# Optimization experiments

Hardware: AMD Instinct MI355X
Metric: run time of the kernel (lower is better)

The kernel has to match this reference:

```python
import jax, jax.numpy as jnp
import numpy as np

G = 32        # grid points per axis (in_p is a regular [0,1]^3 grid)
M = 8         # half n_modes (n_modes=16 -> keep 8 low + 8 high per dim, 8 in rfft dim)
NL = 4        # fno_n_layers
HID = 64      # fno_hidden_channels
LIFT = 256    # fno_lifting_channels
NOUT = 16384  # number of output query points
RADIUS = 0.033


def setup_inputs() -> dict:
    key = jax.random.key(0)
    ks = jax.random.split(key, 16)
    g = jnp.linspace(0.0, 1.0, G)
    X, Y, Z = jnp.meshgrid(g, g, g, indexing='ij')
    in_p = jnp.stack([X, Y, Z], -1).astype(jnp.float32)            # [G,G,G,3]
    f = jax.random.normal(ks[0], (G, G, G, 3), jnp.float32)        # [G,G,G,3]
    out_p = jax.random.uniform(ks[1], (NOUT, 3), dtype=jnp.float32)

    def lin(k, i, o):
        return jax.random.normal(k, (i, o), jnp.float32) * (float(i) ** -0.5)

    inp = {
        'in_p': in_p, 'out_p': out_p, 'f': f,
        # Lifting MLP: (in_channels+3)=6 -> 256 -> 64
        'lift_w1': lin(ks[2], 6, LIFT), 'lift_b1': jnp.zeros((LIFT,), jnp.float32),
        'lift_w2': lin(ks[3], LIFT, HID), 'lift_b2': jnp.zeros((HID,), jnp.float32),
        # Spectral weights: [layer, corner(4), in, out, M, M, M, (re,im)]
        'spec_w': jax.random.normal(ks[4], (NL, 4, HID, HID, M, M, M, 2), jnp.float32) * 0.02,
        # Linear (soft) skip per layer
        'skip_w': jax.random.normal(ks[5], (NL, HID, HID), jnp.float32) * (float(HID) ** -0.5),
        'skip_b': jnp.zeros((NL, HID), jnp.float32),
        # GNO kernel MLP: 6 -> 512 -> 256 -> 64
        'gno_w1': lin(ks[6], 6, 512), 'gno_b1': jnp.zeros((512,), jnp.float32),
        'gno_w2': lin(ks[7], 512, 256), 'gno_b2': jnp.zeros((256,), jnp.float32),
        'gno_w3': lin(ks[8], 256, HID), 'gno_b3': jnp.zeros((HID,), jnp.float32),
        # Projection: 64 -> 256 -> 1
        'proj_w1': lin(ks[9], HID, 256), 'proj_b1': jnp.zeros((256,), jnp.float32),
        'proj_w2': lin(ks[10], 256, 1), 'proj_b2': jnp.zeros((1,), jnp.float32),
    }
    return inp


def reference(in_p, out_p, f, lift_w1, lift_b1, lift_w2, lift_b2, spec_w,
              skip_w, skip_b, gno_w1, gno_b1, gno_w2, gno_b2, gno_w3, gno_b3,
              proj_w1, proj_b1, proj_w2, proj_b2):
    gelu = lambda x: jax.nn.gelu(x, approximate=False)

    # ---- FNO latent embedding (channels-last) ----
    h = jnp.concatenate([f, in_p], -1)                               # [G,G,G,6]
    h = gelu(h @ lift_w1 + lift_b1) @ lift_w2 + lift_b2              # [G,G,G,HID]

    w = spec_w[..., 0] + 1j * spec_w[..., 1]                         # [NL,4,i,o,M,M,M]
    lo, hi = slice(0, M), slice(-M, None)
    corners = [(lo, lo), (lo, hi), (hi, lo), (hi, hi)]
    sz = slice(0, M)
    for l in range(NL):
        ft = jnp.fft.rfftn(h, axes=(0, 1, 2), norm='forward')        # [G,G,G//2+1,HID]
        out_ft = jnp.zeros_like(ft)
        for c, (sx, sy) in enumerate(corners):
            blk = jnp.einsum('xyzi,ioxyz->xyzo', ft[sx, sy, sz], w[l, c])
            out_ft = out_ft.at[sx, sy, sz].set(blk)
        hs = jnp.fft.irfftn(out_ft, s=(G, G, G), axes=(0, 1, 2), norm='forward')
        h = hs + h @ skip_w[l] + skip_b[l]
        if l < NL - 1:
            h = gelu(h)
    latent = h.reshape(-1, HID)                                      # [G^3, HID]

    # ---- GNO: radius neighbor search on regular grid + gather-MLP-mean ----
    hgrid = 1.0 / (G - 1)
    i0 = jnp.round(out_p * (G - 1)).astype(jnp.int32)                # nearest cell [N,3]
    off = jnp.stack(jnp.meshgrid(*([jnp.arange(-1, 2)] * 3), indexing='ij'), -1).reshape(-1, 3)
    cand = i0[:, None, :] + off[None]                                # [N,27,3]
    inb = jnp.all((cand >= 0) & (cand < G), -1)
    cc = jnp.clip(cand, 0, G - 1)
    flat = (cc[..., 0] * G + cc[..., 1]) * G + cc[..., 2]            # [N,27]
    ycoord = cc.astype(jnp.float32) * hgrid                          # neighbor coords
    d2 = jnp.sum((out_p[:, None, :] - ycoord) ** 2, -1)
    mask = inb & (d2 <= RADIUS * RADIUS)

    # kernel input = cat([y_coords, x_coords]) per edge -> MLP -> k(x,y) [N,27,HID]
    agg = jnp.concatenate([ycoord, jnp.broadcast_to(out_p[:, None, :], ycoord.shape)], -1)
    k = gelu(agg @ gno_w1 + gno_b1)
    k = gelu(k @ gno_w2 + gno_b2)
    k = k @ gno_w3 + gno_b3
    fy = latent[flat]                                                # gather [N,27,HID]
    msk = mask[..., None].astype(k.dtype)
    num = jnp.sum(k * fy * msk, axis=1)
    den = jnp.maximum(jnp.sum(msk, axis=1), 1.0)
    out = num / den                                                  # [N,HID] (mean reduce)

    # ---- Projection ----
    out = gelu(out @ proj_w1 + proj_b1) @ proj_w2 + proj_b2          # [N,1]
    return out
```

## Files before the change

kernel.cpp:

```cpp
#include <hip/hip_runtime.h>
#include <math.h>


#define ECAP 131072

typedef _Float16 f16x8 __attribute__((ext_vector_type(8)));
typedef float f32x4 __attribute__((ext_vector_type(4)));

__device__ __forceinline__ float gelu_f(float x) {
    float t = fabsf(x) * 0.7071067811865475f;
    float k = __builtin_amdgcn_rcpf(1.0f + 0.3275911f * t);
    float e = __expf(-t * t);
    float y = k*(0.254829592f + k*(-0.284496736f + k*(1.421413741f +
              k*(-1.453152027f + k*1.061405429f))));
    float erfv = 1.0f - y * e;
    return 0.5f * x * (1.0f + copysignf(erfv, x));
}

__global__ __launch_bounds__(256) void k_prep_w(const float* __restrict__ w2,
                                                const float* __restrict__ w3,
                                                const float* __restrict__ w1,
                                                const float* __restrict__ b1,
                                                const float* __restrict__ lw2,
                                                _Float16* __restrict__ w2T,
                                                _Float16* __restrict__ w3T,
                                                _Float16* __restrict__ w1p,
                                                _Float16* __restrict__ l2hi,
                                                _Float16* __restrict__ l2lo)
{
    int idx = blockIdx.x*256 + threadIdx.x;
    if (idx < 131072) {
        int k = idx >> 8, n = idx & 255;
        w2T[n*512 + k] = (_Float16)w2[idx];
    } else if (idx < 147456) {
        int j = idx - 131072;
        int k = j >> 6, o = j & 63;
        w3T[o*256 + k] = (_Float16)w3[j];
    } else if (idx < 151552) {
        int j = idx - 147456;
        int k = j >> 3, d = j & 7;
        float v = d < 6 ? w1[d*512 + k] : (d == 6 ? b1[k] : 0.0f);
        w1p[k*8 + d] = (_Float16)v;
    } else if (idx < 167936) {
        int j = idx - 151552;
        int o = j >> 8, k = j & 255;
        float v = lw2[k*64 + o];
        _Float16 hi = (_Float16)v;
        l2hi[j] = hi;
        l2lo[j] = (_Float16)(v - (float)hi);
    }
}

__global__ __launch_bounds__(256) void k_lift(
    const float* __restrict__ f, const float* __restrict__ in_p,
    const float* __restrict__ w1, const float* __restrict__ b1,
    const _Float16* __restrict__ l2hi,
    const _Float16* __restrict__ l2lo,
    const float* __restrict__ b2,
    float* __restrict__ h)
{
    __shared__ __align__(16) _Float16 h1hi[64*264];
    __shared__ __align__(16) _Float16 h1lo[64*264];
    __shared__ float w1s[6*256];
    __shared__ float b1s[256];
    float* oT = (float*)h1hi;
    int t = threadIdx.x;
    for (int i = t; i < 1536; i += 256) w1s[i] = w1[i];
    b1s[t] = b1[t];
    int p0 = blockIdx.x * 64;
    int pt = t >> 2, jq = t & 3;
    int p = p0 + pt;
    float x0 = f[p*3+0], x1 = f[p*3+1], x2 = f[p*3+2];
    float x3 = in_p[p*3+0], x4 = in_p[p*3+1], x5 = in_p[p*3+2];
    __syncthreads();
    for (int r = 0; r < 8; ++r) {
        int j0 = jq*64 + r*8;
        f16x8 vh, vl;
        #pragma unroll
        for (int jj = 0; jj < 8; ++jj) {
            int j = j0 + jj;
            float a = b1s[j] + x0*w1s[j] + x1*w1s[256+j] + x2*w1s[512+j]
                    + x3*w1s[768+j] + x4*w1s[1024+j] + x5*w1s[1280+j];
            float g = gelu_f(a);
            _Float16 hi = (_Float16)g;
            vh[jj] = hi;
            vl[jj] = (_Float16)(g - (float)hi);
        }
        *(f16x8*)&h1hi[pt*264 + j0] = vh;
        *(f16x8*)&h1lo[pt*264 + j0] = vl;
    }
    __syncthreads();
    int w = t >> 6, lane = t & 63, l15 = lane & 15, g = lane >> 4;
    f32x4 acc[4];
    #pragma unroll
    for (int nt = 0; nt < 4; ++nt) {
        float bb = b2[nt*16 + l15];
        acc[nt] = (f32x4){bb, bb, bb, bb};
    }
    for (int kk = 0; kk < 8; ++kk) {
        f16x8 ah = *(const f16x8*)&h1hi[(w*16+l15)*264 + kk*32 + g*8];
        f16x8 al = *(const f16x8*)&h1lo[(w*16+l15)*264 + kk*32 + g*8];
        #pragma unroll
        for (int nt = 0; nt < 4; ++nt) {
            f16x8 bh = *(const f16x8*)&l2hi[(nt*16+l15)*256 + kk*32 + g*8];
            f16x8 bl = *(const f16x8*)&l2lo[(nt*16+l15)*256 + kk*32 + g*8];
            acc[nt] = __builtin_amdgcn_mfma_f32_16x16x32_f16(al, bh, acc[nt], 0, 0, 0);
            acc[nt] = __builtin_amdgcn_mfma_f32_16x16x32_f16(ah, bl, acc[nt], 0, 0, 0);
            acc[nt] = __builtin_amdgcn_mfma_f32_16x16x32_f16(ah, bh, acc[nt], 0, 0, 0);
        }
    }
    __syncthreads();
    #pragma unroll
    for (int nt = 0; nt < 4; ++nt)
        #pragma unroll
        for (int r = 0; r < 4; ++r)
            oT[(nt*16 + l15)*68 + w*16 + g*4 + r] = acc[nt][r];
    __syncthreads();
    for (int i = t; i < 4096; i += 256) {
        int c = i >> 6, ptl = i & 63;
        h[(size_t)c*32768 + p0 + ptl] = oT[c*68 + ptl];
    }
}

__global__ __launch_bounds__(256) void k_fwd_zy(const float* __restrict__ h,
                                                float2* __restrict__ F1)
{
    __shared__ float pl[8*1056];
    __shared__ float2 fz[32*73];
    __shared__ float twc[32], tws[32];
    int t = threadIdx.x;
    int x = blockIdx.x >> 3, cg = blockIdx.x & 7;
    for (int i = t; i < 8192; i += 256) {
        int c = i >> 10, yz = i & 1023;
        pl[c*1056 + (yz>>5)*33 + (yz&31)] = h[(cg*8 + c)*32768 + x*1024 + yz];
    }
    if (t < 32) { float th = (float)t*(6.283185307179586f/32.f); twc[t]=cosf(th); tws[t]=sinf(th); }
    __syncthreads();
    {
        int c = t >> 5, y = t & 31;
        float zv[32];
        #pragma unroll
        for (int z = 0; z < 32; ++z) zv[z] = pl[c*1056 + y*33 + z];
        const float inv = 1.0f/32768.0f;
        #pragma unroll
        for (int kz = 0; kz < 8; ++kz) {
            float re = 0.f, im = 0.f;
            #pragma unroll
            for (int z = 0; z < 32; ++z) {
                int ph = (kz*z)&31;
                re += zv[z]*twc[ph];
                im -= zv[z]*tws[ph];
            }
            fz[y*73 + kz*9 + c] = make_float2(re*inv, im*inv);
        }
    }
    __syncthreads();
    #pragma unroll
    for (int ko = 0; ko < 4; ++ko) {
        int idx = ko*256 + t;
        int kyi = idx >> 6, kz = (idx >> 3) & 7, c = idx & 7;
        int ky = kyi < 8 ? kyi : kyi + 16;
        float re = 0.f, im = 0.f;
        for (int y = 0; y < 32; ++y) {
            int ph = (ky*y)&31;
            float cc = twc[ph], ss = tws[ph];
            float2 a = fz[y*73 + kz*9 + c];
            re += a.x*cc + a.y*ss;
            im += a.y*cc - a.x*ss;
        }
        F1[((kyi*8 + kz)*32 + x)*64 + cg*8 + c] = make_float2(re, im);
    }
}

__global__ __launch_bounds__(256) void k_fwd_x(const float2* __restrict__ F1,
                                               float2* __restrict__ Ft)
{
    __shared__ float2 fs[32*65];
    __shared__ float twc[32], tws[32];
    int t = threadIdx.x;
    int kyi = blockIdx.x >> 3, kz = blockIdx.x & 7;
    const float2* src = &F1[(size_t)((kyi*8 + kz)*32)*64];
    for (int i = t; i < 2048; i += 256) fs[(i>>6)*65 + (i&63)] = src[i];
    if (t < 32) { float th = (float)t*(6.283185307179586f/32.f); twc[t]=cosf(th); tws[t]=sinf(th); }
    __syncthreads();
    #pragma unroll
    for (int ko = 0; ko < 4; ++ko) {
        int idx = ko*256 + t;
        int kxi = idx >> 6, ii = idx & 63;
        int kx = kxi < 8 ? kxi : kxi + 16;
        float re = 0.f, im = 0.f;
        for (int xx = 0; xx < 32; ++xx) {
            int ph = (kx*xx)&31;
            float cc = twc[ph], ss = tws[ph];
            float2 a = fs[xx*65 + ii];
            re += a.x*cc + a.y*ss;
            im += a.y*cc - a.x*ss;
        }
        Ft[((kxi*16 + kyi)*8 + kz)*64 + ii] = make_float2(re, im);
    }
}

__global__ __launch_bounds__(256) void k_spec(const float2* __restrict__ Ft,
                                              const float* __restrict__ spw,
                                              float2* __restrict__ Gt, int l)
{
    __shared__ float2 ft2[64*65];
    int t = threadIdx.x;
    int og8 = blockIdx.x >> 5, corner = (blockIdx.x >> 3) & 3, mx = blockIdx.x & 7;
    int kxi = mx + (corner >> 1)*8;
    int kyB = (corner & 1)*8;
    {
        int m = t >> 2, iq = t & 3;
        int my = m >> 3, mz = m & 7;
        int rho = (m >> 1) + ((m & 1) << 5);
        const float2* src = &Ft[(size_t)((kxi*16 + kyB + my)*8 + mz)*64];
        #pragma unroll
        for (int ii = 0; ii < 16; ++ii) {
            int i = iq*16 + ii;
            ft2[rho*65 + i] = src[i];
        }
    }
    __syncthreads();
    int mp = t & 31, oq = t >> 5;
    int o = og8*8 + oq;
    int m0 = 2*mp;
    size_t wbase = (size_t)(l*4 + corner)*4194304 + (size_t)o*1024
                 + (size_t)mx*128 + m0*2;
    float ar0 = 0.f, ai0 = 0.f, ar1 = 0.f, ai1 = 0.f;
    for (int i8 = 0; i8 < 64; i8 += 8) {
        float4 wv[8];
        #pragma unroll
        for (int u = 0; u < 8; ++u)
            wv[u] = *(const float4*)&spw[wbase + (size_t)(i8+u)*65536];
        #pragma unroll
        for (int u = 0; u < 8; ++u) {
            float2 f0 = ft2[mp*65 + i8 + u];
            float2 f1 = ft2[(32 + mp)*65 + i8 + u];
            ar0 += f0.x*wv[u].x - f0.y*wv[u].y;
            ai0 += f0.x*wv[u].y + f0.y*wv[u].x;
            ar1 += f1.x*wv[u].z - f1.y*wv[u].w;
            ai1 += f1.x*wv[u].w + f1.y*wv[u].z;
        }
    }
    size_t gbase = (size_t)(o >> 2)*8192 + (size_t)(corner*8 + mx)*256 + (o & 3);
    Gt[gbase + (size_t)m0*4]       = make_float2(ar0, ai0);
    Gt[gbase + (size_t)(m0+1)*4]   = make_float2(ar1, ai1);
}

__global__ __launch_bounds__(256) void k_inv_skip(const float2* __restrict__ Gt,
                                                  const float* __restrict__ hold,
                                                  const float* __restrict__ skw,
                                                  const float* __restrict__ skb,
                                                  float* __restrict__ hnew,
                                                  float* __restrict__ latent,
                                                  int l)
{
    __shared__ float2 gt[8192];
    __shared__ float2 s1[16*8*4];
    __shared__ float2 s2[32*8*4];
    __shared__ float  skws[256];
    __shared__ float twc[32], tws[32];
    int t = threadIdx.x;
    int x = blockIdx.x >> 4, og = blockIdx.x & 15;
    const float2* gsrc = &Gt[(size_t)og*8192];
    for (int i = t; i < 8192; i += 256) gt[i] = gsrc[i];
    skws[t] = skw[l*4096 + (t>>2)*64 + og*4 + (t&3)];
    if (t < 32) { float th = (float)t*(6.283185307179586f/32.f); twc[t]=cosf(th); tws[t]=sinf(th); }
    __syncthreads();
    #pragma unroll
    for (int ko = 0; ko < 2; ++ko) {
        int idx = ko*256 + t;
        int kyi = idx >> 5, kz = (idx >> 2) & 7, o = idx & 3;
        int cy = kyi >> 3, my = kyi & 7;
        float re = 0.f, im = 0.f;
        #pragma unroll
        for (int cxh = 0; cxh < 2; ++cxh) {
            int corner = cxh*2 + cy;
            #pragma unroll
            for (int mxx = 0; mxx < 8; ++mxx) {
                int kxi = cxh*8 + mxx;
                int kx = kxi < 8 ? kxi : kxi + 16;
                int ph = (kx * x) & 31;
                float cc = twc[ph], ss = tws[ph];
                float2 a = gt[((corner*8 + mxx)*64 + my*8 + kz)*4 + o];
                re += a.x*cc - a.y*ss;
                im += a.x*ss + a.y*cc;
            }
        }
        s1[(kyi*8 + kz)*4 + o] = make_float2(re, im);
    }
    __syncthreads();
    #pragma unroll
    for (int ko = 0; ko < 4; ++ko) {
        int idx = ko*256 + t;
        int y = idx >> 5, kz = (idx >> 2) & 7, o = idx & 3;
        float re = 0.f, im = 0.f;
        #pragma unroll
        for (int kyi = 0; kyi < 16; ++kyi) {
            int ky = kyi < 8 ? kyi : kyi + 16;
            int ph = (ky*y) & 31;
            float cc = twc[ph], ss = tws[ph];
            float2 a = s1[(kyi*8 + kz)*4 + o];
            re += a.x*cc - a.y*ss;
            im += a.x*ss + a.y*cc;
        }
        s2[(y*8 + kz)*4 + o] = make_float2(re, im);
    }
    __syncthreads();
    float acc[4][4];
    #pragma unroll
    for (int pp = 0; pp < 4; ++pp)
        #pragma unroll
        for (int o = 0; o < 4; ++o) acc[pp][o] = skb[l*64 + og*4 + o];
    const float* hsrc = &hold[x*1024 + t*4];
    for (int i = 0; i < 64; ++i) {
        float4 hv = *(const float4*)&hsrc[(size_t)i*32768];
        #pragma unroll
        for (int o = 0; o < 4; ++o) {
            float wv = skws[i*4 + o];
            acc[0][o] += hv.x*wv; acc[1][o] += hv.y*wv;
            acc[2][o] += hv.z*wv; acc[3][o] += hv.w*wv;
        }
    }
    float outv[4][4];
    #pragma unroll
    for (int pp = 0; pp < 4; ++pp) {
        int pt = t*4 + pp;
        int y = pt >> 5, z = pt & 31;
        #pragma unroll
        for (int o = 0; o < 4; ++o) {
            float s = s2[(y*8)*4 + o].x;
            #pragma unroll
            for (int kz = 1; kz < 8; ++kz) {
                int ph = (kz*z) & 31;
                float2 a = s2[(y*8 + kz)*4 + o];
                s += 2.0f*(a.x*twc[ph] - a.y*tws[ph]);
            }
            float v = s + acc[pp][o];
            outv[pp][o] = (l < 3) ? gelu_f(v) : v;
        }
    }
    if (l < 3) {
        #pragma unroll
        for (int o = 0; o < 4; ++o) {
            float4 w4 = make_float4(outv[0][o], outv[1][o], outv[2][o], outv[3][o]);
            *(float4*)&hnew[(size_t)(og*4 + o)*32768 + x*1024 + t*4] = w4;
        }
    } else {
        #pragma unroll
        for (int pp = 0; pp < 4; ++pp) {
            float4 w4 = make_float4(outv[pp][0], outv[pp][1], outv[pp][2], outv[pp][3]);
            *(float4*)&latent[(size_t)(x*1024 + t*4 + pp)*64 + og*4] = w4;
        }
    }
}

__global__ __launch_bounds__(256) void k_gno_build(const float* __restrict__ out_p,
                                                   int* __restrict__ counter,
                                                   int* __restrict__ baseG,
                                                   int* __restrict__ cntG,
                                                   int* __restrict__ eFlat,
                                                   float* __restrict__ eAgg)
{
    int n = blockIdx.x*256 + threadIdx.x;
    const float hg = 1.0f/31.0f;
    const float r2 = (float)(0.033*0.033);
    float px = out_p[n*3+0], py = out_p[n*3+1], pz = out_p[n*3+2];
    int ix = (int)rintf(px*31.f), iy = (int)rintf(py*31.f), iz = (int)rintf(pz*31.f);
    unsigned msk = 0; int cnt = 0;
    for (int j = 0; j < 27; ++j) {
        int dx = j/9 - 1, dy = (j/3)%3 - 1, dz = j%3 - 1;
        int cx = ix+dx, cy = iy+dy, cz = iz+dz;
        bool inb = (cx>=0)&&(cx<32)&&(cy>=0)&&(cy<32)&&(cz>=0)&&(cz<32);
        int qx = min(max(cx,0),31), qy = min(max(cy,0),31), qz = min(max(cz,0),31);
        float yx = qx*hg, yy = qy*hg, yz = qz*hg;
        float d2 = (px-yx)*(px-yx) + (py-yy)*(py-yy) + (pz-yz)*(pz-yz);
        if (inb && d2 <= r2) { msk |= 1u<<j; cnt++; }
    }
    int base = atomicAdd(counter, cnt);
    baseG[n] = base; cntG[n] = cnt;
    int k = 0;
    for (int j = 0; j < 27; ++j) if (msk & (1u<<j)) {
        int dx = j/9 - 1, dy = (j/3)%3 - 1, dz = j%3 - 1;
        int cx = ix+dx, cy = iy+dy, cz = iz+dz;
        int e = base + k;
        eFlat[e] = (cx*32 + cy)*32 + cz;
        eAgg[e*6+0] = cx*hg; eAgg[e*6+1] = cy*hg; eAgg[e*6+2] = cz*hg;
        eAgg[e*6+3] = px;    eAgg[e*6+4] = py;    eAgg[e*6+5] = pz;
        ++k;
    }
}

__global__ __launch_bounds__(256, 2) void k_gno_mlp(
    const int* __restrict__ counter,
    const int* __restrict__ eFlat,
    const float* __restrict__ eAgg,
    const _Float16* __restrict__ w1p,
    const _Float16* __restrict__ w2T,
    const float* __restrict__ b2,
    const _Float16* __restrict__ w3T,
    const float* __restrict__ b3,
    const float* __restrict__ latent,
    float* __restrict__ kv)
{
    __shared__ __align__(16) _Float16 h1pool[64*520];
    __shared__ __align__(16) _Float16 w1s[512*8];
    __shared__ float aggs[64][6];
    __shared__ int   flatS[64];
    _Float16* h2h = h1pool;

    int t = threadIdx.x;
    int E = counter[0]; if (E > ECAP) E = ECAP;
    int s = blockIdx.x * 64;
    if (s >= E) return;
    int ne = min(64, E - s);

    for (int i = t; i < 512; i += 256)
        ((int4*)w1s)[i] = ((const int4*)w1p)[i];
    for (int i = t; i < 384; i += 256)
        aggs[i/6][i - (i/6)*6] = (i < ne*6) ? eAgg[(size_t)s*6 + i] : 0.0f;
    if (t < 64) flatS[t] = (t < ne) ? eFlat[s + t] : 0;
    __syncthreads();

    int e = t & 63;
    int w = t >> 6;
    {
        float a0 = aggs[e][0], a1 = aggs[e][1], a2 = aggs[e][2];
        float a3 = aggs[e][3], a4 = aggs[e][4], a5 = aggs[e][5];
        int xk = (e >> 3) & 7;
        #pragma unroll
        for (int ci = 0; ci < 16; ++ci) {
            int c = w*16 + ci;
            f16x8 v;
            #pragma unroll
            for (int jj = 0; jj < 8; ++jj) {
                int k = c*8 + jj;
                f16x8 wv = *(const f16x8*)&w1s[k*8];
                float pre = (float)wv[6]
                    + a0*(float)wv[0] + a1*(float)wv[1] + a2*(float)wv[2]
                    + a3*(float)wv[3] + a4*(float)wv[4] + a5*(float)wv[5];
                v[jj] = (_Float16)gelu_f(pre);
            }
            *(f16x8*)&h1pool[e*520 + ((c ^ xk)*8)] = v;
        }
    }
    __syncthreads();

    int lane = t & 63;
    int l15 = lane & 15, g = lane >> 4;

    f32x4 acc2[4][4];
    #pragma unroll
    for (int nt = 0; nt < 4; ++nt) {
        float bb = b2[w*64 + nt*16 + l15];
        #pragma unroll
        for (int mt = 0; mt < 4; ++mt) acc2[mt][nt] = (f32x4){bb, bb, bb, bb};
    }
    #pragma unroll 4
    for (int kk = 0; kk < 16; ++kk) {
        f16x8 af[4];
        #pragma unroll
        for (int mt = 0; mt < 4; ++mt) {
            int ee = mt*16 + l15;
            af[mt] = *(const f16x8*)&h1pool[ee*520 + (((kk*4 + g) ^ ((ee>>3)&7))*8)];
        }
        #pragma unroll
        for (int nt = 0; nt < 4; ++nt) {
            f16x8 bf = *(const f16x8*)&w2T[(size_t)(w*64 + nt*16 + l15)*512 + kk*32 + g*8];
            #pragma unroll
            for (int mt = 0; mt < 4; ++mt)
                acc2[mt][nt] = __builtin_amdgcn_mfma_f32_16x16x32_f16(af[mt], bf, acc2[mt][nt], 0, 0, 0);
        }
    }
    __syncthreads();
    #pragma unroll
    for (int mt = 0; mt < 4; ++mt)
      #pragma unroll
      for (int nt = 0; nt < 4; ++nt) {
        int n = w*64 + nt*16 + l15;
        #pragma unroll
        for (int r = 0; r < 4; ++r) {
            int m = mt*16 + g*4 + r;
            h2h[m*264 + (((n>>3) ^ (m&7))*8) + (n&7)] = (_Float16)gelu_f(acc2[mt][nt][r]);
        }
      }
    __syncthreads();

    int o = w*16 + l15;
    f32x4 acc3[4];
    { float bb = b3[o];
      #pragma unroll
      for (int mt = 0; mt < 4; ++mt) acc3[mt] = (f32x4){bb, bb, bb, bb}; }
    #pragma unroll 2
    for (int kk2 = 0; kk2 < 8; ++kk2) {
        f16x8 bf = *(const f16x8*)&w3T[(size_t)o*256 + kk2*32 + g*8];
        #pragma unroll
        for (int mt = 0; mt < 4; ++mt) {
            int ee = mt*16 + l15;
            f16x8 af = *(const f16x8*)&h2h[ee*264 + (((kk2*4 + g) ^ (ee&7))*8)];
            acc3[mt] = __builtin_amdgcn_mfma_f32_16x16x32_f16(af, bf, acc3[mt], 0, 0, 0);
        }
    }

    #pragma unroll
    for (int mt = 0; mt < 4; ++mt) {
        #pragma unroll
        for (int r = 0; r < 4; ++r) {
            int ee = mt*16 + g*4 + r;
            if (ee < ne) {
                float fy = latent[(size_t)flatS[ee]*64 + o];
                kv[(size_t)(s + ee)*64 + o] = acc3[mt][r] * fy;
            }
        }
    }
}

__global__ __launch_bounds__(256) void k_gno_reduce(const int* __restrict__ baseG,
                                                    const int* __restrict__ cntG,
                                                    const float* __restrict__ kv,
                                                    float* __restrict__ num)
{
    int t = threadIdx.x;
    int p = blockIdx.x*16 + (t >> 4);
    int cg = t & 15;
    int base = baseG[p], cnt = cntG[p];
    float4 acc = make_float4(0.f, 0.f, 0.f, 0.f);
    for (int j = 0; j < cnt; ++j) {
        float4 v = *(const float4*)&kv[(size_t)(base + j)*64 + cg*4];
        acc.x += v.x; acc.y += v.y; acc.z += v.z; acc.w += v.w;
    }
    float inv = 1.0f / fmaxf((float)cnt, 1.0f);
    acc.x *= inv; acc.y *= inv; acc.z *= inv; acc.w *= inv;
    *(float4*)&num[(size_t)p*64 + cg*4] = acc;
}

__global__ __launch_bounds__(256) void k_project(const float* __restrict__ num,
                                                 const float* __restrict__ pw1,
                                                 const float* __restrict__ pb1,
                                                 const float* __restrict__ pw2,
                                                 const float* __restrict__ pb2,
                                                 float* __restrict__ outp)
{
    __shared__ float w1s[64*260];
    __shared__ float xT[64*68];
    __shared__ float w2s[256];
    __shared__ float b1s[256];
    __shared__ float red[64*4];
    int t = threadIdx.x;
    int p0 = blockIdx.x * 64;
    for (int i = t; i < 16384; i += 256) {
        int k = i >> 8, o = i & 255;
        w1s[k*260 + o] = pw1[i];
    }
    w2s[t] = pw2[t];
    b1s[t] = pb1[t];
    for (int i = t; i < 4096; i += 256) {
        int ptl = i >> 6, c = i & 63;
        xT[c*68 + ptl] = num[(size_t)(p0 + ptl)*64 + c];
    }
    __syncthreads();
    int pr = t & 15, oc0 = t >> 4;
    float psum[4] = {0.f, 0.f, 0.f, 0.f};
    for (int it = 0; it < 4; ++it) {
        int oc = it*16 + oc0;
        float a[4][4];
        #pragma unroll
        for (int pp = 0; pp < 4; ++pp)
            #pragma unroll
            for (int q = 0; q < 4; ++q) a[pp][q] = b1s[oc*4 + q];
        for (int i = 0; i < 64; ++i) {
            float4 xv = *(const float4*)&xT[i*68 + pr*4];
            float4 wv = *(const float4*)&w1s[i*260 + oc*4];
            #pragma unroll
            for (int q = 0; q < 4; ++q) {
                float wq = (&wv.x)[q];
                a[0][q] += xv.x*wq; a[1][q] += xv.y*wq;
                a[2][q] += xv.z*wq; a[3][q] += xv.w*wq;
            }
        }
        #pragma unroll
        for (int pp = 0; pp < 4; ++pp) {
            float s = 0.f;
            #pragma unroll
            for (int q = 0; q < 4; ++q) s += gelu_f(a[pp][q]) * w2s[oc*4 + q];
            psum[pp] += s;
        }
    }
    #pragma unroll
    for (int pp = 0; pp < 4; ++pp) {
        psum[pp] += __shfl_xor(psum[pp], 16, 64);
        psum[pp] += __shfl_xor(psum[pp], 32, 64);
    }
    int lane = t & 63, w = t >> 6;
    if (lane < 16) {
        #pragma unroll
        for (int pp = 0; pp < 4; ++pp) red[(lane*4 + pp)*4 + w] = psum[pp];
    }
    __syncthreads();
    if (t < 64)
        outp[p0 + t] = red[t*4+0] + red[t*4+1] + red[t*4+2] + red[t*4+3] + pb2[0];
}

extern "C" void kernel_launch(void* const* d_in, const int* in_sizes, int n_in,
                              void* d_out, int out_size, void* d_ws, size_t ws_size,
                              hipStream_t stream)
{
    const float* in_p = (const float*)d_in[0];
    const float* outp = (const float*)d_in[1];
    const float* f    = (const float*)d_in[2];
    const float* lw1  = (const float*)d_in[3];
    const float* lb1  = (const float*)d_in[4];
    const float* lw2  = (const float*)d_in[5];
    const float* lb2  = (const float*)d_in[6];
    const float* spw  = (const float*)d_in[7];
    const float* skw  = (const float*)d_in[8];
    const float* skb  = (const float*)d_in[9];
    const float* gw1  = (const float*)d_in[10];
    const float* gb1  = (const float*)d_in[11];
    const float* gw2  = (const float*)d_in[12];
    const float* gb2  = (const float*)d_in[13];
    const float* gw3  = (const float*)d_in[14];
    const float* gb3  = (const float*)d_in[15];
    const float* pw1  = (const float*)d_in[16];
    const float* pb1  = (const float*)d_in[17];
    const float* pw2  = (const float*)d_in[18];
    const float* pb2  = (const float*)d_in[19];

    float* ws   = (float*)d_ws;
    float* buf0 = ws;
    float* buf1 = ws + 2097152;
    float* SC   = ws + 4194304;
    float2* F1 = (float2*)SC;
    float2* Ft = (float2*)(SC + 524288);
    float2* Gt = (float2*)(SC + 786432);
    float* numb = SC;
    _Float16* w2T  = (_Float16*)(SC + 1048576);
    _Float16* w3T  = (_Float16*)(SC + 1114112);
    _Float16* w1p  = (_Float16*)(SC + 1122304);
    _Float16* l2hi = (_Float16*)(SC + 1124352);
    _Float16* l2lo = (_Float16*)(SC + 1132544);
    int*   counter = (int*)(SC + 1140736);
    int*   baseG   = (int*)(SC + 1140752);
    int*   cntG    = (int*)(SC + 1157136);
    int*   eFlat   = (int*)(SC + 1173520);
    float* eAgg    = SC + 1304592;
    float* kv      = SC + 2091024;

    k_prep_w<<<656, 256, 0, stream>>>(gw2, gw3, gw1, gb1, lw2,
                                      w2T, w3T, w1p, l2hi, l2lo);
    k_lift<<<512, 256, 0, stream>>>(f, in_p, lw1, lb1, l2hi, l2lo, lb2, buf0);

    hipMemsetAsync(counter, 0, sizeof(int), stream);
    k_gno_build<<<64, 256, 0, stream>>>(outp, counter, baseG, cntG, eFlat, eAgg);

    for (int l = 0; l < 4; ++l) {
        const float* hin = (l & 1) ? buf1 : buf0;
        float* hout = (l & 1) ? buf0 : buf1;
        k_fwd_zy<<<256, 256, 0, stream>>>(hin, F1);
        k_fwd_x<<<128, 256, 0, stream>>>(F1, Ft);
        k_spec<<<256, 256, 0, stream>>>(Ft, spw, Gt, l);
        k_inv_skip<<<512, 256, 0, stream>>>(Gt, hin, skw, skb, hout, buf0, l);
    }

    k_gno_mlp<<<ECAP/64, 256, 0, stream>>>(counter, eFlat, eAgg,
                                           w1p, w2T, gb2, w3T, gb3, buf0, kv);
    k_gno_reduce<<<1024, 256, 0, stream>>>(baseG, cntG, kv, numb);
    k_project<<<256, 256, 0, stream>>>(numb, pw1, pb1, pw2, pb2, (float*)d_out);
}
```

Measured before the change: 417.6 us.

## Fuse GNO build into prep, MFMA skip matmul in spectral kernel, merge reduce into projection

Moves the per-layer skip linear (64x64 over 32768 points) out of the inverse-FFT kernel into extra blocks of the spectral kernel. These blocks use fp16 hi/lo split MFMA so the skip product runs concurrently with the spectral contraction, and the inverse kernel only adds the precomputed skip result. GNO neighbour building is folded into the weight-prep launch, and the GNO mean reduction is folded into the projection kernel, removing two launches and the intermediate num buffer. The cost is an extra hsk round-trip through global memory per layer and a slightly different numerical path for the skip (three-term fp16 split).

```diff
diff --git a/kernel.cpp b/kernel.cpp
--- a/kernel.cpp
+++ b/kernel.cpp
@@ -17,17 +17,56 @@
     return 0.5f * x * (1.0f + copysignf(erfv, x));
 }
 
-__global__ __launch_bounds__(256) void k_prep_w(const float* __restrict__ w2,
-                                                const float* __restrict__ w3,
-                                                const float* __restrict__ w1,
-                                                const float* __restrict__ b1,
-                                                const float* __restrict__ lw2,
-                                                _Float16* __restrict__ w2T,
-                                                _Float16* __restrict__ w3T,
-                                                _Float16* __restrict__ w1p,
-                                                _Float16* __restrict__ l2hi,
-                                                _Float16* __restrict__ l2lo)
-{
+__global__ __launch_bounds__(256) void k_prep(const float* __restrict__ w2,
+                                              const float* __restrict__ w3,
+                                              const float* __restrict__ w1,
+                                              const float* __restrict__ b1,
+                                              const float* __restrict__ lw2,
+                                              const float* __restrict__ skw,
+                                              const float* __restrict__ out_p,
+                                              _Float16* __restrict__ w2T,
+                                              _Float16* __restrict__ w3T,
+                                              _Float16* __restrict__ w1p,
+                                              _Float16* __restrict__ l2hi,
+                                              _Float16* __restrict__ l2lo,
+                                              _Float16* __restrict__ skwH,
+                                              _Float16* __restrict__ skwL,
+                                              int* __restrict__ counter,
+                                              int* __restrict__ baseG,
+                                              int* __restrict__ cntG,
+                                              int* __restrict__ eFlat,
+                                              float* __restrict__ eAgg)
+{
+    if (blockIdx.x >= 720) {
+        int n = (blockIdx.x - 720)*256 + threadIdx.x;
+        const float hg = 1.0f/31.0f;
+        const float r2 = (float)(0.033*0.033);
+        float px = out_p[n*3+0], py = out_p[n*3+1], pz = out_p[n*3+2];
+        int ix = (int)rintf(px*31.f), iy = (int)rintf(py*31.f), iz = (int)rintf(pz*31.f);
+        unsigned msk = 0; int cnt = 0;
+        for (int j = 0; j < 27; ++j) {
+            int dx = j/9 - 1, dy = (j/3)%3 - 1, dz = j%3 - 1;
+            int cx = ix+dx, cy = iy+dy, cz = iz+dz;
+            bool inb = (cx>=0)&&(cx<32)&&(cy>=0)&&(cy<32)&&(cz>=0)&&(cz<32);
+            int qx = min(max(cx,0),31), qy = min(max(cy,0),31), qz = min(max(cz,0),31);
+            float yx = qx*hg, yy = qy*hg, yz = qz*hg;
+            float d2 = (px-yx)*(px-yx) + (py-yy)*(py-yy) + (pz-yz)*(pz-yz);
+            if (inb && d2 <= r2) { msk |= 1u<<j; cnt++; }
+        }
+        int base = atomicAdd(counter, cnt);
+        baseG[n] = base; cntG[n] = cnt;
+        int k = 0;
+        for (int j = 0; j < 27; ++j) if (msk & (1u<<j)) {
+            int dx = j/9 - 1, dy = (j/3)%3 - 1, dz = j%3 - 1;
+            int cx = ix+dx, cy = iy+dy, cz = iz+dz;
+            int e = base + k;
+            eFlat[e] = (cx*32 + cy)*32 + cz;
+            eAgg[e*6+0] = cx*hg; eAgg[e*6+1] = cy*hg; eAgg[e*6+2] = cz*hg;
+            eAgg[e*6+3] = px;    eAgg[e*6+4] = py;    eAgg[e*6+5] = pz;
+            ++k;
+        }
+        return;
+    }
     int idx = blockIdx.x*256 + threadIdx.x;
     if (idx < 131072) {
         int k = idx >> 8, n = idx & 255;
@@ -48,6 +87,14 @@
         _Float16 hi = (_Float16)v;
         l2hi[j] = hi;
         l2lo[j] = (_Float16)(v - (float)hi);
+    } else if (idx < 184320) {
+        int j = idx - 167936;
+        int l = j >> 12, r = j & 4095;
+        int co = r >> 6, ci = r & 63;
+        float v = skw[l*4096 + ci*64 + co];
+        _Float16 hi = (_Float16)v;
+        skwH[j] = hi;
+        skwL[j] = (_Float16)(v - (float)hi);
     }
 }
 
@@ -200,12 +247,57 @@
     }
 }
 
-__global__ __launch_bounds__(256) void k_spec(const float2* __restrict__ Ft,
-                                              const float* __restrict__ spw,
-                                              float2* __restrict__ Gt, int l)
+__global__ __launch_bounds__(256) void k_spec_skip(const float2* __restrict__ Ft,
+                                                   const float* __restrict__ spw,
+                                                   const float* __restrict__ hold,
+                                                   const _Float16* __restrict__ skwH,
+                                                   const _Float16* __restrict__ skwL,
+                                                   float2* __restrict__ Gt,
+                                                   float* __restrict__ hsk,
+                                                   int l)
 {
     __shared__ float2 ft2[64*65];
+    __shared__ __align__(16) _Float16 shi[128*72];
+    __shared__ __align__(16) _Float16 slo[128*72];
     int t = threadIdx.x;
+    if (blockIdx.x >= 256) {
+        int pt0 = (blockIdx.x - 256) * 128;
+        for (int i = t; i < 2048; i += 256) {
+            int ci = i >> 5, q = i & 31;
+            float4 v = *(const float4*)&hold[(size_t)ci*32768 + pt0 + q*4];
+            #pragma unroll
+            for (int j = 0; j < 4; ++j) {
+                float fv = (&v.x)[j];
+                _Float16 hi = (_Float16)fv;
+                shi[(q*4+j)*72 + ci] = hi;
+                slo[(q*4+j)*72 + ci] = (_Float16)(fv - (float)hi);
+            }
+        }
+        __syncthreads();
+        int w = t >> 6, lane = t & 63, l15 = lane & 15, g = lane >> 4;
+        f32x4 acc[8];
+        #pragma unroll
+        for (int nt = 0; nt < 8; ++nt) acc[nt] = (f32x4){0.f, 0.f, 0.f, 0.f};
+        #pragma unroll
+        for (int kk = 0; kk < 2; ++kk) {
+            f16x8 ah = *(const f16x8*)&skwH[l*4096 + (w*16+l15)*64 + kk*32 + g*8];
+            f16x8 al = *(const f16x8*)&skwL[l*4096 + (w*16+l15)*64 + kk*32 + g*8];
+            #pragma unroll
+            for (int nt = 0; nt < 8; ++nt) {
+                f16x8 bh = *(const f16x8*)&shi[(nt*16+l15)*72 + kk*32 + g*8];
+                f16x8 bl = *(const f16x8*)&slo[(nt*16+l15)*72 + kk*32 + g*8];
+                acc[nt] = __builtin_amdgcn_mfma_f32_16x16x32_f16(al, bh, acc[nt], 0, 0, 0);
+                acc[nt] = __builtin_amdgcn_mfma_f32_16x16x32_f16(ah, bl, acc[nt], 0, 0, 0);
+                acc[nt] = __builtin_amdgcn_mfma_f32_16x16x32_f16(ah, bh, acc[nt], 0, 0, 0);
+            }
+        }
+        #pragma unroll
+        for (int nt = 0; nt < 8; ++nt)
+            #pragma unroll
+            for (int r = 0; r < 4; ++r)
+                hsk[(size_t)(w*16 + g*4 + r)*32768 + pt0 + nt*16 + l15] = acc[nt][r];
+        return;
+    }
     int og8 = blockIdx.x >> 5, corner = (blockIdx.x >> 3) & 3, mx = blockIdx.x & 7;
     int kxi = mx + (corner >> 1)*8;
     int kyB = (corner & 1)*8;
@@ -247,24 +339,21 @@
     Gt[gbase + (size_t)(m0+1)*4]   = make_float2(ar1, ai1);
 }
 
-__global__ __launch_bounds__(256) void k_inv_skip(const float2* __restrict__ Gt,
-                                                  const float* __restrict__ hold,
-                                                  const float* __restrict__ skw,
-                                                  const float* __restrict__ skb,
-                                                  float* __restrict__ hnew,
-                                                  float* __restrict__ latent,
-                                                  int l)
+__global__ __launch_bounds__(256) void k_inv(const float2* __restrict__ Gt,
+                                             const float* __restrict__ hsk,
+                                             const float* __restrict__ skb,
+                                             float* __restrict__ hnew,
+                                             float* __restrict__ latent,
+                                             int l)
 {
     __shared__ float2 gt[8192];
     __shared__ float2 s1[16*8*4];
     __shared__ float2 s2[32*8*4];
-    __shared__ float  skws[256];
     __shared__ float twc[32], tws[32];
     int t = threadIdx.x;
     int x = blockIdx.x >> 4, og = blockIdx.x & 15;
     const float2* gsrc = &Gt[(size_t)og*8192];
     for (int i = t; i < 8192; i += 256) gt[i] = gsrc[i];
-    skws[t] = skw[l*4096 + (t>>2)*64 + og*4 + (t&3)];
     if (t < 32) { float th = (float)t*(6.283185307179586f/32.f); twc[t]=cosf(th); tws[t]=sinf(th); }
     __syncthreads();
     #pragma unroll
@@ -309,18 +398,11 @@
     __syncthreads();
     float acc[4][4];
     #pragma unroll
-    for (int pp = 0; pp < 4; ++pp)
-        #pragma unroll
-        for (int o = 0; o < 4; ++o) acc[pp][o] = skb[l*64 + og*4 + o];
-    const float* hsrc = &hold[x*1024 + t*4];
-    for (int i = 0; i < 64; ++i) {
-        float4 hv = *(const float4*)&hsrc[(size_t)i*32768];
-        #pragma unroll
-        for (int o = 0; o < 4; ++o) {
-            float wv = skws[i*4 + o];
-            acc[0][o] += hv.x*wv; acc[1][o] += hv.y*wv;
-            acc[2][o] += hv.z*wv; acc[3][o] += hv.w*wv;
-        }
+    for (int o = 0; o < 4; ++o) {
+        float bb = skb[l*64 + og*4 + o];
+        float4 hv = *(const float4*)&hsk[(size_t)(og*4+o)*32768 + x*1024 + t*4];
+        acc[0][o] = bb + hv.x; acc[1][o] = bb + hv.y;
+        acc[2][o] = bb + hv.z; acc[3][o] = bb + hv.w;
     }
     float outv[4][4];
     #pragma unroll
@@ -352,42 +434,6 @@
             float4 w4 = make_float4(outv[pp][0], outv[pp][1], outv[pp][2], outv[pp][3]);
             *(float4*)&latent[(size_t)(x*1024 + t*4 + pp)*64 + og*4] = w4;
         }
-    }
-}
-
-__global__ __launch_bounds__(256) void k_gno_build(const float* __restrict__ out_p,
-                                                   int* __restrict__ counter,
-                                                   int* __restrict__ baseG,
-                                                   int* __restrict__ cntG,
-                                                   int* __restrict__ eFlat,
-                                                   float* __restrict__ eAgg)
-{
-    int n = blockIdx.x*256 + threadIdx.x;
-    const float hg = 1.0f/31.0f;
-    const float r2 = (float)(0.033*0.033);
-    float px = out_p[n*3+0], py = out_p[n*3+1], pz = out_p[n*3+2];
-    int ix = (int)rintf(px*31.f), iy = (int)rintf(py*31.f), iz = (int)rintf(pz*31.f);
-    unsigned msk = 0; int cnt = 0;
-    for (int j = 0; j < 27; ++j) {
-        int dx = j/9 - 1, dy = (j/3)%3 - 1, dz = j%3 - 1;
-        int cx = ix+dx, cy = iy+dy, cz = iz+dz;
-        bool inb = (cx>=0)&&(cx<32)&&(cy>=0)&&(cy<32)&&(cz>=0)&&(cz<32);
-        int qx = min(max(cx,0),31), qy = min(max(cy,0),31), qz = min(max(cz,0),31);
-        float yx = qx*hg, yy = qy*hg, yz = qz*hg;
-        float d2 = (px-yx)*(px-yx) + (py-yy)*(py-yy) + (pz-yz)*(pz-yz);
-        if (inb && d2 <= r2) { msk |= 1u<<j; cnt++; }
-    }
-    int base = atomicAdd(counter, cnt);
-    baseG[n] = base; cntG[n] = cnt;
-    int k = 0;
-    for (int j = 0; j < 27; ++j) if (msk & (1u<<j)) {
-        int dx = j/9 - 1, dy = (j/3)%3 - 1, dz = j%3 - 1;
-        int cx = ix+dx, cy = iy+dy, cz = iz+dz;
-        int e = base + k;
-        eFlat[e] = (cx*32 + cy)*32 + cz;
-        eAgg[e*6+0] = cx*hg; eAgg[e*6+1] = cy*hg; eAgg[e*6+2] = cz*hg;
-        eAgg[e*6+3] = px;    eAgg[e*6+4] = py;    eAgg[e*6+5] = pz;
-        ++k;
     }
 }
 
@@ -515,26 +561,9 @@
     }
 }
 
-__global__ __launch_bounds__(256) void k_gno_reduce(const int* __restrict__ baseG,
-                                                    const int* __restrict__ cntG,
-                                                    const float* __restrict__ kv,
-                                                    float* __restrict__ num)
-{
-    int t = threadIdx.x;
-    int p = blockIdx.x*16 + (t >> 4);
-    int cg = t & 15;
-    int base = baseG[p], cnt = cntG[p];
-    float4 acc = make_float4(0.f, 0.f, 0.f, 0.f);
-    for (int j = 0; j < cnt; ++j) {
-        float4 v = *(const float4*)&kv[(size_t)(base + j)*64 + cg*4];
-        acc.x += v.x; acc.y += v.y; acc.z += v.z; acc.w += v.w;
-    }
-    float inv = 1.0f / fmaxf((float)cnt, 1.0f);
-    acc.x *= inv; acc.y *= inv; acc.z *= inv; acc.w *= inv;
-    *(float4*)&num[(size_t)p*64 + cg*4] = acc;
-}
-
-__global__ __launch_bounds__(256) void k_project(const float* __restrict__ num,
+__global__ __launch_bounds__(256) void k_project(const int* __restrict__ baseG,
+                                                 const int* __restrict__ cntG,
+                                                 const float* __restrict__ kv,
                                                  const float* __restrict__ pw1,
                                                  const float* __restrict__ pb1,
                                                  const float* __restrict__ pw2,
@@ -556,7 +585,11 @@
     b1s[t] = pb1[t];
     for (int i = t; i < 4096; i += 256) {
         int ptl = i >> 6, c = i & 63;
-        xT[c*68 + ptl] = num[(size_t)(p0 + ptl)*64 + c];
+        int p = p0 + ptl;
+        int base = baseG[p], cnt = cntG[p];
+        float acc = 0.f;
+        for (int j = 0; j < cnt; ++j) acc += kv[(size_t)(base + j)*64 + c];
+        xT[c*68 + ptl] = acc / fmaxf((float)cnt, 1.0f);
     }
     __syncthreads();
     int pr = t & 15, oc0 = t >> 4;
@@ -633,37 +666,38 @@
     float2* F1 = (float2*)SC;
     float2* Ft = (float2*)(SC + 524288);
     float2* Gt = (float2*)(SC + 786432);
-    float* numb = SC;
     _Float16* w2T  = (_Float16*)(SC + 1048576);
     _Float16* w3T  = (_Float16*)(SC + 1114112);
     _Float16* w1p  = (_Float16*)(SC + 1122304);
     _Float16* l2hi = (_Float16*)(SC + 1124352);
     _Float16* l2lo = (_Float16*)(SC + 1132544);
-    int*   counter = (int*)(SC + 1140736);
-    int*   baseG   = (int*)(SC + 1140752);
-    int*   cntG    = (int*)(SC + 1157136);
-    int*   eFlat   = (int*)(SC + 1173520);
-    float* eAgg    = SC + 1304592;
-    float* kv      = SC + 2091024;
-
-    k_prep_w<<<656, 256, 0, stream>>>(gw2, gw3, gw1, gb1, lw2,
-                                      w2T, w3T, w1p, l2hi, l2lo);
+    _Float16* skwH = (_Float16*)(SC + 1140736);
+    _Float16* skwL = (_Float16*)(SC + 1148928);
+    int*   counter = (int*)(SC + 1157120);
+    int*   baseG   = (int*)(SC + 1157136);
+    int*   cntG    = (int*)(SC + 1173520);
+    int*   eFlat   = (int*)(SC + 1189904);
+    float* eAgg    = SC + 1320976;
+    float* kv      = SC + 2107408;
+    float* hsk     = SC + 10496016;
+
+    hipMemsetAsync(counter, 0, sizeof(int), stream);
+    k_prep<<<784, 256, 0, stream>>>(gw2, gw3, gw1, gb1, lw2, skw, outp,
+                                    w2T, w3T, w1p, l2hi, l2lo, skwH, skwL,
+                                    counter, baseG, cntG, eFlat, eAgg);
     k_lift<<<512, 256, 0, stream>>>(f, in_p, lw1, lb1, l2hi, l2lo, lb2, buf0);
-
-    hipMemsetAsync(counter, 0, sizeof(int), stream);
-    k_gno_build<<<64, 256, 0, stream>>>(outp, counter, baseG, cntG, eFlat, eAgg);
 
     for (int l = 0; l < 4; ++l) {
         const float* hin = (l & 1) ? buf1 : buf0;
         float* hout = (l & 1) ? buf0 : buf1;
         k_fwd_zy<<<256, 256, 0, stream>>>(hin, F1);
         k_fwd_x<<<128, 256, 0, stream>>>(F1, Ft);
-        k_spec<<<256, 256, 0, stream>>>(Ft, spw, Gt, l);
-        k_inv_skip<<<512, 256, 0, stream>>>(Gt, hin, skw, skb, hout, buf0, l);
+        k_spec_skip<<<512, 256, 0, stream>>>(Ft, spw, hin, skwH, skwL, Gt, hsk, l);
+        k_inv<<<512, 256, 0, stream>>>(Gt, hsk, skb, hout, buf0, l);
     }
 
     k_gno_mlp<<<ECAP/64, 256, 0, stream>>>(counter, eFlat, eAgg,
                                            w1p, w2T, gb2, w3T, gb3, buf0, kv);
-    k_gno_reduce<<<1024, 256, 0, stream>>>(baseG, cntG, kv, numb);
-    k_project<<<256, 256, 0, stream>>>(numb, pw1, pb1, pw2, pb2, (float*)d_out);
-}
+    k_project<<<256, 256, 0, stream>>>(baseG, cntG, kv, pw1, pb1, pw2, pb2,
+                                       (float*)d_out);
+}
```

New measurement: 415.7 us. Within noise of the previous version (-0.5%).
